# Kernel optimization log

Measured on AMD Instinct MI355X. Metric: run time of the kernel, lower is better.

Reference implementation:

```python
import jax, jax.numpy as jnp
import numpy as np

DIM = 1024
H = 16
DH = 64
INTER = H * DH

def setup_inputs() -> dict:
    key = jax.random.key(0)
    k1, k2, k3, k4 = jax.random.split(key, 4)
    input = jax.random.normal(k1, (4, 2048, DIM), dtype=jnp.float32)
    # nn.Linear weights stored as [out, in]; we keep [in, out] for x @ W
    W_qkv = jax.random.normal(k2, (DIM, INTER * 3), dtype=jnp.float32) * 0.02
    W_mlp = jax.random.normal(k3, (INTER, DIM), dtype=jnp.float32) * 0.02
    b_mlp = jax.random.normal(k4, (DIM,), dtype=jnp.float32) * 0.02
    return {"input": input, "W_qkv": W_qkv, "W_mlp": W_mlp, "b_mlp": b_mlp}

def reference(input, W_qkv, W_mlp, b_mlp):
    b, n, _ = input.shape
    qkv = input @ W_qkv                      # [b, n, 3*h*d]
    qkv = qkv.reshape(b, n, 3, H, DH)        # matches '(qkv h d)' split order
    qkv = jnp.transpose(qkv, (2, 0, 3, 1, 4))  # [3, b, h, n, d]
    q, k, v = qkv[0], qkv[1], qkv[2]
    scale = DH ** -0.5
    attn = jnp.einsum('bhnd,bhmd->bhnm', q, k) * scale
    attn = jax.nn.softmax(attn, axis=-1)
    out = jnp.einsum('bhnm,bhmd->bhnd', attn, v)
    out = jnp.transpose(out, (0, 2, 1, 3)).reshape(b, n, INTER)  # 'b h n d -> b n (h d)'
    return out @ W_mlp + b_mlp
```

## Files before the change

kernel.cpp:

```cpp
#include <hip/hip_runtime.h>
#include <stdint.h>

typedef __attribute__((ext_vector_type(8))) short bf16x8;
typedef __attribute__((ext_vector_type(4))) float f32x4;
typedef __attribute__((ext_vector_type(16))) float f32x16;

#define MFMA16(a, b, c) __builtin_amdgcn_mfma_f32_16x16x32_bf16((a), (b), (c), 0, 0, 0)
#define MFMA32(a, b, c) __builtin_amdgcn_mfma_f32_32x32x16_bf16((a), (b), (c), 0, 0, 0)

__device__ __forceinline__ unsigned short f2bf(float x) {
  uint32_t u = __float_as_uint(x);
  u += 0x7fffu + ((u >> 16) & 1u);
  return (unsigned short)(u >> 16);
}

__device__ __forceinline__ uint32_t cvt_pk_bf16(float a, float b) {
  uint32_t r;
  asm("v_cvt_pk_bf16_f32 %0, %1, %2" : "=v"(r) : "v"(a), "v"(b));
  return r;
}

__device__ __forceinline__ float exp2_hw(float x) {
  float r;
  asm("v_exp_f32 %0, %1" : "=v"(r) : "v"(x));
  return r;
}

__device__ __forceinline__ void gload_lds16(const void* g, void* l) {
  __builtin_amdgcn_global_load_lds(
      (const __attribute__((address_space(1))) uint32_t*)g,
      (__attribute__((address_space(3))) uint32_t*)l, 16, 0, 0);
}

__global__ __launch_bounds__(256) void prep_kernel(
    const float* __restrict__ X, unsigned short* __restrict__ Xb,
    const float* __restrict__ Wq, unsigned short* __restrict__ Wqt,
    const float* __restrict__ Wm, unsigned short* __restrict__ Wmt) {
  __shared__ float tile[64][65];
  const int bid = blockIdx.x;
  const int t = threadIdx.x;
  if (bid < 4096) {
    const int i = bid * 256 + t;
    const float4 a = *(const float4*)(X + (size_t)i * 8);
    const float4 b = *(const float4*)(X + (size_t)i * 8 + 4);
    uint4 o;
    o.x = (uint32_t)f2bf(a.x) | ((uint32_t)f2bf(a.y) << 16);
    o.y = (uint32_t)f2bf(a.z) | ((uint32_t)f2bf(a.w) << 16);
    o.z = (uint32_t)f2bf(b.x) | ((uint32_t)f2bf(b.y) << 16);
    o.w = (uint32_t)f2bf(b.z) | ((uint32_t)f2bf(b.w) << 16);
    *(uint4*)(Xb + (size_t)i * 8) = o;
    return;
  }
  const float* src;
  unsigned short* dst;
  int Nd, lb;
  if (bid < 4864) { src = Wq; dst = Wqt; Nd = 3072; lb = bid - 4096; }
  else            { src = Wm; dst = Wmt; Nd = 1024; lb = bid - 4864; }
  const int Kd = 1024;
  const int ntc = Nd >> 6;
  const int r0 = (lb / ntc) << 6;
  const int c0 = (lb % ntc) << 6;
  const int tr = t >> 4;
  const int tc4 = (t & 15) << 2;
#pragma unroll
  for (int p = 0; p < 4; ++p) {
    int row = p * 16 + tr;
    float4 v = *(const float4*)(src + (size_t)(r0 + row) * Nd + c0 + tc4);
    tile[row][tc4 + 0] = v.x;
    tile[row][tc4 + 1] = v.y;
    tile[row][tc4 + 2] = v.z;
    tile[row][tc4 + 3] = v.w;
  }
  __syncthreads();
#pragma unroll
  for (int p = 0; p < 4; ++p) {
    int c = p * 16 + tr;
    int r4 = (t & 15) << 2;
    uint2 pv;
    pv.x = (uint32_t)f2bf(tile[r4 + 0][c]) | ((uint32_t)f2bf(tile[r4 + 1][c]) << 16);
    pv.y = (uint32_t)f2bf(tile[r4 + 2][c]) | ((uint32_t)f2bf(tile[r4 + 3][c]) << 16);
    *(uint2*)(dst + (size_t)(c0 + c) * Kd + r0 + r4) = pv;
  }
}

__global__ __launch_bounds__(512, 2) void gemm_qkv_kernel(
    const unsigned short* __restrict__ A,
    const unsigned short* __restrict__ Bt,
    unsigned short* __restrict__ Qo,
    unsigned short* __restrict__ Ko,
    unsigned short* __restrict__ Vo) {
  constexpr int Kdim = 1024, BK = 64;
  __shared__ __align__(16) unsigned short lds_pool[49152];
#define LA(nb) (lds_pool + (nb) * 8192)
#define LB(nb) (lds_pool + 16384 + (nb) * 16384)
  const int nbn = 12;
  const int wg = (blockIdx.x & 7) * 96 + (blockIdx.x >> 3);
  const int bi = wg / nbn, bj = wg % nbn;
  const int tid = threadIdx.x;
  const int l = tid & 63, wid = tid >> 6;
  const int wr = wid >> 2, wc = wid & 3;
  const int lr = l & 15, lg = l >> 4;

  const f32x4 vzero = {0.f, 0.f, 0.f, 0.f};
  f32x4 acc[4][4];
#pragma unroll
  for (int i = 0; i < 4; ++i)
#pragma unroll
    for (int j = 0; j < 4; ++j) acc[i][j] = vzero;

  const int srow = tid >> 3;
  const int sc = tid & 7;
  const int sg = sc ^ (srow & 7);
  const unsigned short* As = A + (size_t)(bi * 128 + srow) * Kdim + sg * 8;
  const unsigned short* Bs = Bt + (size_t)(bj * 256 + srow) * Kdim + sg * 8;

#define STAGE_T(nb, kt)                                                           \
  {                                                                               \
    const int k0_ = (kt) * BK;                                                    \
    gload_lds16(As + k0_,                     &LA(nb)[(srow) * BK + sc * 8]);     \
    gload_lds16(As + (size_t)64 * Kdim + k0_,  &LA(nb)[(srow + 64) * BK + sc * 8]);\
    gload_lds16(Bs + k0_,                     &LB(nb)[(srow) * BK + sc * 8]);     \
    gload_lds16(Bs + (size_t)64 * Kdim + k0_,  &LB(nb)[(srow + 64) * BK + sc * 8]);\
    gload_lds16(Bs + (size_t)128 * Kdim + k0_, &LB(nb)[(srow + 128) * BK + sc * 8]);\
    gload_lds16(Bs + (size_t)192 * Kdim + k0_, &LB(nb)[(srow + 192) * BK + sc * 8]);\
  }

  STAGE_T(0, 0);
  asm volatile("s_waitcnt vmcnt(0)" ::: "memory");
  __builtin_amdgcn_s_barrier();

  for (int T = 0; T < 16; ++T) {
    const int cur = T & 1;
    bf16x8 bfr[4][2], af[2][2];
#pragma unroll
    for (int jt = 0; jt < 4; ++jt) {
      const int r = wc * 64 + jt * 16 + lr;
#pragma unroll
      for (int kk = 0; kk < 2; ++kk)
        bfr[jt][kk] = *(const bf16x8*)&LB(cur)[r * BK + (((kk * 4 + lg) ^ (r & 7)) * 8)];
    }
#pragma unroll
    for (int it = 0; it < 2; ++it) {
      const int r = wr * 64 + it * 16 + lr;
#pragma unroll
      for (int kk = 0; kk < 2; ++kk)
        af[it][kk] = *(const bf16x8*)&LA(cur)[r * BK + (((kk * 4 + lg) ^ (r & 7)) * 8)];
    }
    if (T < 15) STAGE_T(cur ^ 1, T + 1);
    __builtin_amdgcn_s_barrier();
    asm volatile("s_waitcnt lgkmcnt(0)" ::: "memory");
    __builtin_amdgcn_sched_barrier(0);
    __builtin_amdgcn_s_setprio(1);
#pragma unroll
    for (int it = 0; it < 2; ++it)
#pragma unroll
      for (int jt = 0; jt < 4; ++jt) {
        acc[it][jt] = MFMA16(af[it][0], bfr[jt][0], acc[it][jt]);
        acc[it][jt] = MFMA16(af[it][1], bfr[jt][1], acc[it][jt]);
      }
    __builtin_amdgcn_s_setprio(0);
    __builtin_amdgcn_s_barrier();

    bf16x8 af2[2][2];
#pragma unroll
    for (int it = 0; it < 2; ++it) {
      const int r = wr * 64 + (it + 2) * 16 + lr;
#pragma unroll
      for (int kk = 0; kk < 2; ++kk)
        af2[it][kk] = *(const bf16x8*)&LA(cur)[r * BK + (((kk * 4 + lg) ^ (r & 7)) * 8)];
    }
    __builtin_amdgcn_s_barrier();
    asm volatile("s_waitcnt lgkmcnt(0)" ::: "memory");
    __builtin_amdgcn_sched_barrier(0);
    __builtin_amdgcn_s_setprio(1);
#pragma unroll
    for (int it = 0; it < 2; ++it)
#pragma unroll
      for (int jt = 0; jt < 4; ++jt) {
        acc[it + 2][jt] = MFMA16(af2[it][0], bfr[jt][0], acc[it + 2][jt]);
        acc[it + 2][jt] = MFMA16(af2[it][1], bfr[jt][1], acc[it + 2][jt]);
      }
    __builtin_amdgcn_s_setprio(0);
    asm volatile("s_waitcnt vmcnt(0)" ::: "memory");
    __builtin_amdgcn_s_barrier();
  }

  const int s = bj >> 2;
  const int h0 = (bj & 3) * 4;
  const int b = (bi * 128) >> 11;
  const int nbase = (bi * 128) & 2047;
  unsigned short* E = lds_pool;
  __syncthreads();
  if (s == 2) {
#pragma unroll
    for (int jt = 0; jt < 4; ++jt) {
      const int cl = wc * 64 + jt * 16 + lr;
      const int hl = cl >> 6, d = cl & 63;
#pragma unroll
      for (int it = 0; it < 4; ++it) {
        const int nl0 = wr * 64 + it * 16 + lg * 4;
#pragma unroll
        for (int rg = 0; rg < 4; ++rg) {
          const int nl = nl0 + rg;
          E[(((nl >> 3) * 4 + hl) * 64 + d) * 8 + (nl & 7)] = f2bf(acc[it][jt][rg]);
        }
      }
    }
  } else {
    const float scl = (s == 0) ? 0.18033688011112042f : 1.0f;
#pragma unroll
    for (int jt = 0; jt < 4; ++jt) {
      const int cl = wc * 64 + jt * 16 + lr;
      const int hl = cl >> 6, d = cl & 63;
#pragma unroll
      for (int it = 0; it < 4; ++it) {
        const int nl0 = wr * 64 + it * 16 + lg * 4;
#pragma unroll
        for (int rg = 0; rg < 4; ++rg)
          E[((nl0 + rg) * 4 + hl) * 64 + d] = f2bf(acc[it][jt][rg] * scl);
      }
    }
  }
  __syncthreads();
  const uint4* Es = (const uint4*)E;
  if (s == 0) {
#pragma unroll
    for (int i = 0; i < 8; ++i) {
      const int c = i * 512 + tid;
      const int dc = c & 7, nl = (c >> 3) & 127, hl = c >> 10;
      const size_t g = ((size_t)(b * 16 + h0 + hl) * 2048 + nbase + nl) * 8 + dc;
      ((uint4*)Qo)[g] = Es[(nl * 4 + hl) * 8 + dc];
    }
  } else if (s == 1) {
#pragma unroll
    for (int i = 0; i < 8; ++i) {
      const int c = i * 512 + tid;
      const int nl = c & 127, cc = (c >> 7) & 7, hl = c >> 10;
      const size_t g = ((size_t)(b * 16 + h0 + hl) * 8 + cc) * 2048 + nbase + nl;
      ((uint4*)Ko)[g] = Es[(nl * 4 + hl) * 8 + cc];
    }
  } else {
    const int ncbase = nbase >> 3;
#pragma unroll
    for (int i = 0; i < 8; ++i) {
      const int c = i * 512 + tid;
      const int d = c & 63, nc = (c >> 6) & 15, hl = c >> 10;
      const size_t g = ((size_t)(b * 16 + h0 + hl) * 256 + ncbase + nc) * 64 + d;
      ((uint4*)Vo)[g] = Es[(nc * 4 + hl) * 64 + d];
    }
  }
#undef STAGE_T
#undef LA
#undef LB
}

template <int T>
__device__ __forceinline__ bf16x8 build_pa(const f32x16& s, int hi) {
  uint32_t A1 = cvt_pk_bf16(s[T * 8 + 0], s[T * 8 + 1]);
  uint32_t A2 = cvt_pk_bf16(s[T * 8 + 2], s[T * 8 + 3]);
  uint32_t B1 = cvt_pk_bf16(s[T * 8 + 4], s[T * 8 + 5]);
  uint32_t B2 = cvt_pk_bf16(s[T * 8 + 6], s[T * 8 + 7]);
  uint32_t send1 = hi ? A1 : B1;
  uint32_t send2 = hi ? A2 : B2;
  uint32_t recv1 = (uint32_t)__shfl_xor((int)send1, 32);
  uint32_t recv2 = (uint32_t)__shfl_xor((int)send2, 32);
  union { uint32_t u[4]; bf16x8 v; } r;
  r.u[0] = hi ? recv1 : A1;
  r.u[1] = hi ? recv2 : A2;
  r.u[2] = hi ? B1 : recv1;
  r.u[3] = hi ? B2 : recv2;
  return r.v;
}

__device__ __forceinline__ float tile_sum(const f32x16& a, const f32x16& b) {
  float st[8];
#pragma unroll
  for (int i = 0; i < 8; ++i) st[i] = (a[i] + a[i + 8]) + (b[i] + b[i + 8]);
  float sm = ((st[0] + st[1]) + (st[2] + st[3])) + ((st[4] + st[5]) + (st[6] + st[7]));
  sm += __shfl_xor(sm, 32);
  return sm;
}

__global__ __launch_bounds__(256, 2) void attn_kernel(
    const unsigned short* __restrict__ Qg,
    const unsigned short* __restrict__ Kg,
    const unsigned short* __restrict__ Vg,
    unsigned short* __restrict__ AO) {
  const int bid = blockIdx.x;
  const int bh = (bid & 7) * 8 + (bid >> 6);
  const int qt = (bid >> 3) & 7;
  const int tid = threadIdx.x;
  const int l = tid & 63, w = tid >> 6;
  const int lo = l & 31, hi = l >> 5;
  const int qb = qt * 256 + w * 64;

  bf16x8 qfA[4], qfB[4];
  {
    const unsigned short* qrowA = Qg + ((size_t)bh * 2048 + qb + lo) * 64 + hi * 8;
    const unsigned short* qrowB = qrowA + 32 * 64;
#pragma unroll
    for (int ds = 0; ds < 4; ++ds) {
      qfA[ds] = *(const bf16x8*)(qrowA + ds * 16);
      qfB[ds] = *(const bf16x8*)(qrowB + ds * 16);
    }
  }

  f32x16 oA0, oA1, oB0, oB1;
#pragma unroll
  for (int i = 0; i < 16; ++i) { oA0[i] = 0.f; oA1[i] = 0.f; oB0[i] = 0.f; oB1[i] = 0.f; }
  float lA_ = 0.f, lB_ = 0.f;

  const unsigned short* Kp = Kg + ((size_t)(bh * 8 + hi) * 2048 + lo) * 8;
  const unsigned short* Vp = Vg + ((size_t)(bh * 256 + hi) * 64 + lo) * 8;

  bf16x8 kf0[4], kf1[4], vf0[4], vf1[4];
#pragma unroll
  for (int ds = 0; ds < 4; ++ds) {
    kf0[ds] = *(const bf16x8*)(Kp + ds * 32768);
    kf1[ds] = *(const bf16x8*)(Kp + ds * 32768 + 256);
  }

  for (int t = 0; t < 32; ++t) {
#pragma unroll
    for (int ks = 0; ks < 4; ++ks) {
      vf0[ks] = *(const bf16x8*)(Vp + (size_t)t * 4096 + ks * 1024);
      vf1[ks] = *(const bf16x8*)(Vp + (size_t)t * 4096 + ks * 1024 + 256);
    }

    f32x16 sA0, sA1, sB0, sB1;
#pragma unroll
    for (int i = 0; i < 16; ++i) { sA0[i] = 0.f; sA1[i] = 0.f; sB0[i] = 0.f; sB1[i] = 0.f; }
    __builtin_amdgcn_s_setprio(1);
#pragma unroll
    for (int ds = 0; ds < 4; ++ds) {
      sA0 = MFMA32(kf0[ds], qfA[ds], sA0);
      sA1 = MFMA32(kf1[ds], qfA[ds], sA1);
      sB0 = MFMA32(kf0[ds], qfB[ds], sB0);
      sB1 = MFMA32(kf1[ds], qfB[ds], sB1);
    }
    __builtin_amdgcn_s_setprio(0);

    if (t < 31) {
#pragma unroll
      for (int ds = 0; ds < 4; ++ds) {
        kf0[ds] = *(const bf16x8*)(Kp + (size_t)(t + 1) * 512 + ds * 32768);
        kf1[ds] = *(const bf16x8*)(Kp + (size_t)(t + 1) * 512 + ds * 32768 + 256);
      }
    }

#pragma unroll
    for (int i = 0; i < 16; ++i) { sA0[i] = exp2_hw(sA0[i]); sA1[i] = exp2_hw(sA1[i]); }
#pragma unroll
    for (int i = 0; i < 16; ++i) { sB0[i] = exp2_hw(sB0[i]); sB1[i] = exp2_hw(sB1[i]); }
    lA_ += tile_sum(sA0, sA1);
    lB_ += tile_sum(sB0, sB1);

    bf16x8 paA[4] = {build_pa<0>(sA0, hi), build_pa<1>(sA0, hi),
                     build_pa<0>(sA1, hi), build_pa<1>(sA1, hi)};
    bf16x8 paB[4] = {build_pa<0>(sB0, hi), build_pa<1>(sB0, hi),
                     build_pa<0>(sB1, hi), build_pa<1>(sB1, hi)};

    __builtin_amdgcn_s_setprio(1);
#pragma unroll
    for (int ks = 0; ks < 4; ++ks) {
      oA0 = MFMA32(vf0[ks], paA[ks], oA0);
      oA1 = MFMA32(vf1[ks], paA[ks], oA1);
      oB0 = MFMA32(vf0[ks], paB[ks], oB0);
      oB1 = MFMA32(vf1[ks], paB[ks], oB1);
    }
    __builtin_amdgcn_s_setprio(0);
  }

  const float linvA = 1.0f / lA_;
  const float linvB = 1.0f / lB_;
  const int b = bh >> 4, h = bh & 15;
  unsigned short* dstA = AO + ((size_t)(b * 2048 + qb + lo) * 1024 + h * 64 + 4 * hi);
  unsigned short* dstB = dstA + (size_t)32 * 1024;
#pragma unroll
  for (int q4 = 0; q4 < 4; ++q4) {
    uint2 p0;
    p0.x = cvt_pk_bf16(oA0[q4 * 4 + 0] * linvA, oA0[q4 * 4 + 1] * linvA);
    p0.y = cvt_pk_bf16(oA0[q4 * 4 + 2] * linvA, oA0[q4 * 4 + 3] * linvA);
    *(uint2*)(dstA + q4 * 8) = p0;
    uint2 p1;
    p1.x = cvt_pk_bf16(oA1[q4 * 4 + 0] * linvA, oA1[q4 * 4 + 1] * linvA);
    p1.y = cvt_pk_bf16(oA1[q4 * 4 + 2] * linvA, oA1[q4 * 4 + 3] * linvA);
    *(uint2*)(dstA + 32 + q4 * 8) = p1;
    uint2 p2;
    p2.x = cvt_pk_bf16(oB0[q4 * 4 + 0] * linvB, oB0[q4 * 4 + 1] * linvB);
    p2.y = cvt_pk_bf16(oB0[q4 * 4 + 2] * linvB, oB0[q4 * 4 + 3] * linvB);
    *(uint2*)(dstB + q4 * 8) = p2;
    uint2 p3;
    p3.x = cvt_pk_bf16(oB1[q4 * 4 + 0] * linvB, oB1[q4 * 4 + 1] * linvB);
    p3.y = cvt_pk_bf16(oB1[q4 * 4 + 2] * linvB, oB1[q4 * 4 + 3] * linvB);
    *(uint2*)(dstB + 32 + q4 * 8) = p3;
  }
}

__global__ __launch_bounds__(256, 2) void gemm_mlp_kernel(
    const unsigned short* __restrict__ A,
    const unsigned short* __restrict__ Bt,
    const float* __restrict__ bias,
    float* __restrict__ out) {
  constexpr int Kdim = 1024, BK = 64;
  __shared__ __align__(16) float pool_f[16384];
  unsigned short* lA = (unsigned short*)pool_f;
  unsigned short* lB = lA + 8192;
  const int nbn = 8;
  const int wg = (blockIdx.x & 7) * 64 + (blockIdx.x >> 3);
  const int bi = wg / nbn, bj = wg % nbn;
  const int tid = threadIdx.x;
  const int l = tid & 63, w = tid >> 6;
  const int wr = w >> 1, wc = w & 1;
  const int lr = l & 15, lg = l >> 4;

  const f32x4 vzero = {0.f, 0.f, 0.f, 0.f};
  f32x4 acc[4][4];
#pragma unroll
  for (int i = 0; i < 4; ++i)
#pragma unroll
    for (int j = 0; j < 4; ++j) acc[i][j] = vzero;

  const int srow = tid >> 3;
  const int sc = tid & 7;
  const int sg = sc ^ (srow & 7);
  const unsigned short* As = A + (size_t)(bi * 128 + srow) * Kdim + sg * 8;
  const unsigned short* Bs = Bt + (size_t)(bj * 128 + srow) * Kdim + sg * 8;
  unsigned short* dA = &lA[(srow * 8 + sc) * 8];
  unsigned short* dB = &lB[(srow * 8 + sc) * 8];

  for (int kt = 0; kt < Kdim / BK; ++kt) {
    const int k0 = kt * BK;
#pragma unroll
    for (int rr = 0; rr < 4; ++rr) {
      gload_lds16(As + (size_t)rr * 32 * Kdim + k0, dA + rr * 32 * BK);
      gload_lds16(Bs + (size_t)rr * 32 * Kdim + k0, dB + rr * 32 * BK);
    }
    __syncthreads();
#pragma unroll
    for (int kk = 0; kk < 2; ++kk) {
      bf16x8 af[4], bfr[4];
#pragma unroll
      for (int it = 0; it < 4; ++it) {
        int r = wr * 64 + it * 16 + lr;
        af[it] = *(const bf16x8*)&lA[r * BK + (((kk * 4 + lg) ^ (lr & 7)) * 8)];
      }
#pragma unroll
      for (int jt = 0; jt < 4; ++jt) {
        int r = wc * 64 + jt * 16 + lr;
        bfr[jt] = *(const bf16x8*)&lB[r * BK + (((kk * 4 + lg) ^ (lr & 7)) * 8)];
      }
#pragma unroll
      for (int it = 0; it < 4; ++it)
#pragma unroll
        for (int jt = 0; jt < 4; ++jt)
          acc[it][jt] = MFMA16(af[it], bfr[jt], acc[it][jt]);
    }
    __syncthreads();
  }

#pragma unroll
  for (int jt = 0; jt < 4; ++jt) {
    const int cl = wc * 64 + jt * 16 + lr;
    const float bv = bias[bj * 128 + cl];
#pragma unroll
    for (int it = 0; it < 4; ++it) {
      const int m0 = wr * 64 + it * 16 + lg * 4;
#pragma unroll
      for (int rg = 0; rg < 4; ++rg)
        pool_f[(m0 + rg) * 128 + cl] = acc[it][jt][rg] + bv;
    }
  }
  __syncthreads();
  const uint4* Ef = (const uint4*)pool_f;
  uint4* Og = (uint4*)out;
#pragma unroll
  for (int i = 0; i < 16; ++i) {
    const int c = i * 256 + tid;
    const int cc = c & 31, m = c >> 5;
    Og[(size_t)(bi * 128 + m) * 256 + bj * 32 + cc] = Ef[m * 32 + cc];
  }
}

extern "C" void kernel_launch(void* const* d_in, const int* in_sizes, int n_in,
                              void* d_out, int out_size, void* d_ws, size_t ws_size,
                              hipStream_t stream) {
  const float* X = (const float*)d_in[0];
  const float* Wqkv = (const float*)d_in[1];
  const float* Wmlp = (const float*)d_in[2];
  const float* bmlp = (const float*)d_in[3];
  float* out = (float*)d_out;

  char* ws = (char*)d_ws;
  unsigned short* Xb  = (unsigned short*)(ws);
  unsigned short* Wqt = (unsigned short*)(ws + 16777216);
  unsigned short* Wmt = (unsigned short*)(ws + 23068672);
  unsigned short* Qb  = (unsigned short*)(ws + 25165824);
  unsigned short* Kb  = (unsigned short*)(ws + 41943040);
  unsigned short* Vb  = (unsigned short*)(ws + 58720256);
  unsigned short* AOb = (unsigned short*)(ws + 75497472);

  prep_kernel<<<5120, 256, 0, stream>>>(X, Xb, Wqkv, Wqt, Wmlp, Wmt);
  gemm_qkv_kernel<<<768, 512, 0, stream>>>(Xb, Wqt, Qb, Kb, Vb);
  attn_kernel<<<512, 256, 0, stream>>>(Qb, Kb, Vb, AOb);
  gemm_mlp_kernel<<<512, 256, 0, stream>>>(AOb, Wmt, bmlp, out);
}
```

Measured before the change: 182.2 us.

## Restructure MLP GEMM into 128x256 tiles with double-buffered LDS pipeline

The output projection GEMM now uses 512-thread blocks computing 128x256 tiles (half as many blocks) and double-buffers A/B tiles in LDS. The next k-tile is prefetched while MFMAs run, and MFMA phases are split into two halves with barriers and s_setprio, following the QKV kernel's schedule. The epilogue writes the wider tile in two passes through the shared LDS pool. This is meant to hide global-load latency and cut redundant A loads, at the cost of 96KB of LDS per block, which may limit occupancy.

```diff
diff --git a/kernel.cpp b/kernel.cpp
--- a/kernel.cpp
+++ b/kernel.cpp
@@ -397,21 +397,21 @@
   }
 }
 
-__global__ __launch_bounds__(256, 2) void gemm_mlp_kernel(
+__global__ __launch_bounds__(512, 2) void gemm_mlp_kernel(
     const unsigned short* __restrict__ A,
     const unsigned short* __restrict__ Bt,
     const float* __restrict__ bias,
     float* __restrict__ out) {
   constexpr int Kdim = 1024, BK = 64;
-  __shared__ __align__(16) float pool_f[16384];
-  unsigned short* lA = (unsigned short*)pool_f;
-  unsigned short* lB = lA + 8192;
-  const int nbn = 8;
-  const int wg = (blockIdx.x & 7) * 64 + (blockIdx.x >> 3);
+  __shared__ __align__(16) unsigned short lds_pool[49152];
+#define LA(nb) (lds_pool + (nb) * 8192)
+#define LB(nb) (lds_pool + 16384 + (nb) * 16384)
+  const int nbn = 4;
+  const int wg = (blockIdx.x & 7) * 32 + (blockIdx.x >> 3);
   const int bi = wg / nbn, bj = wg % nbn;
   const int tid = threadIdx.x;
-  const int l = tid & 63, w = tid >> 6;
-  const int wr = w >> 1, wc = w & 1;
+  const int l = tid & 63, wid = tid >> 6;
+  const int wr = wid >> 2, wc = wid & 3;
   const int lr = l & 15, lg = l >> 4;
 
   const f32x4 vzero = {0.f, 0.f, 0.f, 0.f};
@@ -425,61 +425,111 @@
   const int sc = tid & 7;
   const int sg = sc ^ (srow & 7);
   const unsigned short* As = A + (size_t)(bi * 128 + srow) * Kdim + sg * 8;
-  const unsigned short* Bs = Bt + (size_t)(bj * 128 + srow) * Kdim + sg * 8;
-  unsigned short* dA = &lA[(srow * 8 + sc) * 8];
-  unsigned short* dB = &lB[(srow * 8 + sc) * 8];
-
-  for (int kt = 0; kt < Kdim / BK; ++kt) {
-    const int k0 = kt * BK;
-#pragma unroll
-    for (int rr = 0; rr < 4; ++rr) {
-      gload_lds16(As + (size_t)rr * 32 * Kdim + k0, dA + rr * 32 * BK);
-      gload_lds16(Bs + (size_t)rr * 32 * Kdim + k0, dB + rr * 32 * BK);
-    }
+  const unsigned short* Bs = Bt + (size_t)(bj * 256 + srow) * Kdim + sg * 8;
+
+#define STAGE_T(nb, kt)                                                           \
+  {                                                                               \
+    const int k0_ = (kt) * BK;                                                    \
+    gload_lds16(As + k0_,                     &LA(nb)[(srow) * BK + sc * 8]);     \
+    gload_lds16(As + (size_t)64 * Kdim + k0_,  &LA(nb)[(srow + 64) * BK + sc * 8]);\
+    gload_lds16(Bs + k0_,                     &LB(nb)[(srow) * BK + sc * 8]);     \
+    gload_lds16(Bs + (size_t)64 * Kdim + k0_,  &LB(nb)[(srow + 64) * BK + sc * 8]);\
+    gload_lds16(Bs + (size_t)128 * Kdim + k0_, &LB(nb)[(srow + 128) * BK + sc * 8]);\
+    gload_lds16(Bs + (size_t)192 * Kdim + k0_, &LB(nb)[(srow + 192) * BK + sc * 8]);\
+  }
+
+  STAGE_T(0, 0);
+  asm volatile("s_waitcnt vmcnt(0)" ::: "memory");
+  __builtin_amdgcn_s_barrier();
+
+  for (int T = 0; T < 16; ++T) {
+    const int cur = T & 1;
+    bf16x8 bfr[4][2], af[2][2];
+#pragma unroll
+    for (int jt = 0; jt < 4; ++jt) {
+      const int r = wc * 64 + jt * 16 + lr;
+#pragma unroll
+      for (int kk = 0; kk < 2; ++kk)
+        bfr[jt][kk] = *(const bf16x8*)&LB(cur)[r * BK + (((kk * 4 + lg) ^ (r & 7)) * 8)];
+    }
+#pragma unroll
+    for (int it = 0; it < 2; ++it) {
+      const int r = wr * 64 + it * 16 + lr;
+#pragma unroll
+      for (int kk = 0; kk < 2; ++kk)
+        af[it][kk] = *(const bf16x8*)&LA(cur)[r * BK + (((kk * 4 + lg) ^ (r & 7)) * 8)];
+    }
+    if (T < 15) STAGE_T(cur ^ 1, T + 1);
+    __builtin_amdgcn_s_barrier();
+    asm volatile("s_waitcnt lgkmcnt(0)" ::: "memory");
+    __builtin_amdgcn_sched_barrier(0);
+    __builtin_amdgcn_s_setprio(1);
+#pragma unroll
+    for (int it = 0; it < 2; ++it)
+#pragma unroll
+      for (int jt = 0; jt < 4; ++jt) {
+        acc[it][jt] = MFMA16(af[it][0], bfr[jt][0], acc[it][jt]);
+        acc[it][jt] = MFMA16(af[it][1], bfr[jt][1], acc[it][jt]);
+      }
+    __builtin_amdgcn_s_setprio(0);
+    __builtin_amdgcn_s_barrier();
+
+    bf16x8 af2[2][2];
+#pragma unroll
+    for (int it = 0; it < 2; ++it) {
+      const int r = wr * 64 + (it + 2) * 16 + lr;
+#pragma unroll
+      for (int kk = 0; kk < 2; ++kk)
+        af2[it][kk] = *(const bf16x8*)&LA(cur)[r * BK + (((kk * 4 + lg) ^ (r & 7)) * 8)];
+    }
+    __builtin_amdgcn_s_barrier();
+    asm volatile("s_waitcnt lgkmcnt(0)" ::: "memory");
+    __builtin_amdgcn_sched_barrier(0);
+    __builtin_amdgcn_s_setprio(1);
+#pragma unroll
+    for (int it = 0; it < 2; ++it)
+#pragma unroll
+      for (int jt = 0; jt < 4; ++jt) {
+        acc[it + 2][jt] = MFMA16(af2[it][0], bfr[jt][0], acc[it + 2][jt]);
+        acc[it + 2][jt] = MFMA16(af2[it][1], bfr[jt][1], acc[it + 2][jt]);
+      }
+    __builtin_amdgcn_s_setprio(0);
+    asm volatile("s_waitcnt vmcnt(0)" ::: "memory");
+    __builtin_amdgcn_s_barrier();
+  }
+
+  float* Ef = (float*)lds_pool;
+  uint4* Og = (uint4*)out;
+#pragma unroll
+  for (int h = 0; h < 2; ++h) {
     __syncthreads();
-#pragma unroll
-    for (int kk = 0; kk < 2; ++kk) {
-      bf16x8 af[4], bfr[4];
-#pragma unroll
-      for (int it = 0; it < 4; ++it) {
-        int r = wr * 64 + it * 16 + lr;
-        af[it] = *(const bf16x8*)&lA[r * BK + (((kk * 4 + lg) ^ (lr & 7)) * 8)];
-      }
+    if ((wc >> 1) == h) {
 #pragma unroll
       for (int jt = 0; jt < 4; ++jt) {
-        int r = wc * 64 + jt * 16 + lr;
-        bfr[jt] = *(const bf16x8*)&lB[r * BK + (((kk * 4 + lg) ^ (lr & 7)) * 8)];
-      }
-#pragma unroll
-      for (int it = 0; it < 4; ++it)
-#pragma unroll
-        for (int jt = 0; jt < 4; ++jt)
-          acc[it][jt] = MFMA16(af[it], bfr[jt], acc[it][jt]);
+        const int cg = wc * 64 + jt * 16 + lr;
+        const int cl = cg - h * 128;
+        const float bv = bias[bj * 256 + cg];
+#pragma unroll
+        for (int it = 0; it < 4; ++it) {
+          const int m0 = wr * 64 + it * 16 + lg * 4;
+#pragma unroll
+          for (int rg = 0; rg < 4; ++rg)
+            Ef[(m0 + rg) * 128 + cl] = acc[it][jt][rg] + bv;
+        }
+      }
     }
     __syncthreads();
-  }
-
-#pragma unroll
-  for (int jt = 0; jt < 4; ++jt) {
-    const int cl = wc * 64 + jt * 16 + lr;
-    const float bv = bias[bj * 128 + cl];
-#pragma unroll
-    for (int it = 0; it < 4; ++it) {
-      const int m0 = wr * 64 + it * 16 + lg * 4;
-#pragma unroll
-      for (int rg = 0; rg < 4; ++rg)
-        pool_f[(m0 + rg) * 128 + cl] = acc[it][jt][rg] + bv;
-    }
-  }
-  __syncthreads();
-  const uint4* Ef = (const uint4*)pool_f;
-  uint4* Og = (uint4*)out;
-#pragma unroll
-  for (int i = 0; i < 16; ++i) {
-    const int c = i * 256 + tid;
-    const int cc = c & 31, m = c >> 5;
-    Og[(size_t)(bi * 128 + m) * 256 + bj * 32 + cc] = Ef[m * 32 + cc];
-  }
+    const uint4* E4 = (const uint4*)Ef;
+#pragma unroll
+    for (int i = 0; i < 8; ++i) {
+      const int c = i * 512 + tid;
+      const int cc = c & 31, m = c >> 5;
+      Og[(size_t)(bi * 128 + m) * 256 + bj * 64 + h * 32 + cc] = E4[m * 32 + cc];
+    }
+  }
+#undef STAGE_T
+#undef LA
+#undef LB
 }
 
 extern "C" void kernel_launch(void* const* d_in, const int* in_sizes, int n_in,
@@ -503,5 +553,5 @@
   prep_kernel<<<5120, 256, 0, stream>>>(X, Xb, Wqkv, Wqt, Wmlp, Wmt);
   gemm_qkv_kernel<<<768, 512, 0, stream>>>(Xb, Wqt, Qb, Kb, Vb);
   attn_kernel<<<512, 256, 0, stream>>>(Qb, Kb, Vb, AOb);
-  gemm_mlp_kernel<<<512, 256, 0, stream>>>(AOb, Wmt, bmlp, out);
-}
+  gemm_mlp_kernel<<<256, 512, 0, stream>>>(AOb, Wmt, bmlp, out);
+}
```

Measured after the change: 183.2 us. About the same (+0.5%).
